# Kernel tuning notes

Hardware: AMD Instinct MI355X
Metric: run time of the kernel (lower is better)

The kernel has to match this reference:

```python
import jax, jax.numpy as jnp
import numpy as np

N_NODES = 500_000
N_EDGES = 2_500_000
N_GRAPHS = 1024


def _linear_params(key, fan_in, fan_out):
    # mimic torch.nn.Linear default init: U(-1/sqrt(fan_in), 1/sqrt(fan_in))
    k1, k2 = jax.random.split(key)
    bound = 1.0 / np.sqrt(fan_in)
    W = jax.random.uniform(k1, (fan_in, fan_out), jnp.float32, -bound, bound)
    b = jax.random.uniform(k2, (fan_out,), jnp.float32, -bound, bound)
    return W, b


def setup_inputs() -> dict:
    key = jax.random.key(0)
    ks = jax.random.split(key, 8)
    x = jax.random.normal(ks[0], (N_NODES, 2), jnp.float32)
    edge_index = jax.random.randint(ks[1], (2, N_EDGES), 0, N_NODES, jnp.int32)
    batch = jnp.sort(jax.random.randint(ks[2], (N_NODES,), 0, N_GRAPHS, jnp.int32))
    W1, b1 = _linear_params(ks[3], 2, 16)
    W2, b2 = _linear_params(ks[4], 16, 32)
    Wf1, bf1 = _linear_params(ks[5], 32, 16)
    Wf2, bf2 = _linear_params(ks[6], 16, 1)
    return {"x": x, "edge_index": edge_index, "batch": batch,
            "W1": W1, "b1": b1, "W2": W2, "b2": b2,
            "Wf1": Wf1, "bf1": bf1, "Wf2": Wf2, "bf2": bf2}


def _gnn_conv(h, W, b, src, dst, n_nodes):
    # Linear then add-aggregate: out[dst] += h_lin[src]  (self-loops already in src/dst)
    h = h @ W + b                       # [N, out]
    msgs = h[src]                       # gather over edges: [E+N, out]
    return jax.ops.segment_sum(msgs, dst, num_segments=n_nodes)


def reference(x, edge_index, batch, W1, b1, W2, b2, Wf1, bf1, Wf2, bf2):
    n = x.shape[0]
    loop = jnp.arange(n, dtype=edge_index.dtype)
    src = jnp.concatenate([edge_index[0], loop])  # source nodes (x_j)
    dst = jnp.concatenate([edge_index[1], loop])  # target nodes (aggregation index)

    h = jax.nn.relu(_gnn_conv(x, W1, b1, src, dst, n))   # [N, 16]
    h = jax.nn.relu(_gnn_conv(h, W2, b2, src, dst, n))   # [N, 32]

    # global mean pool per graph
    sums = jax.ops.segment_sum(h, batch, num_segments=N_GRAPHS)           # [G, 32]
    cnts = jax.ops.segment_sum(jnp.ones((n, 1), h.dtype), batch, num_segments=N_GRAPHS)
    pooled = sums / jnp.maximum(cnts, 1.0)

    out = jax.nn.relu(pooled @ Wf1 + bf1)
    out = out @ Wf2 + bf2                                # [G, 1]
    return out
```

## Files before the change

### kernel.cpp

```cpp
#include <hip/hip_runtime.h>


#define TPB 256
#define SBK_BITS 9
#define SBK 512
#define NSBX 1024
#define CAPX 576
#define CAPS 3072
#define PE1 4096

typedef unsigned int uint32;

__device__ __forceinline__ float reluf(float v) { return v > 0.f ? v : 0.f; }

__global__ void kPart1(const int* __restrict__ src, const int* __restrict__ dst,
                       int* __restrict__ curx, int* __restrict__ part1x, int E) {
    __shared__ int h[NSBX];
    for (int i = threadIdx.x; i < NSBX; i += TPB) h[i] = 0;
    __syncthreads();
    int base = blockIdx.x * PE1;
    int end = base + PE1 < E ? base + PE1 : E;
    for (int e = base + threadIdx.x; e < end; e += TPB)
        atomicAdd(&h[dst[e] >> SBK_BITS], 1);
    __syncthreads();
    int slice = blockIdx.x & 7;
    int* cur = curx + slice * NSBX;
    int rbase = slice * (NSBX * CAPX);
    for (int i = threadIdx.x; i < NSBX; i += TPB) {
        int c = h[i];
        if (c) h[i] = i * CAPX + atomicAdd(&cur[i], c);
    }
    __syncthreads();
    for (int e = base + threadIdx.x; e < end; e += TPB) {
        int d = dst[e];
        int b = d >> SBK_BITS;
        int pos = atomicAdd(&h[b], 1);
        if (pos < (b + 1) * CAPX)
            part1x[rbase + pos] = (src[e] << SBK_BITS) | (d & (SBK - 1));
    }
}

__global__ void kPart2C1(const int* __restrict__ curx, const int* __restrict__ part1x,
                         const float* __restrict__ x,
                         int* __restrict__ rowptr, int* __restrict__ supEnd,
                         int* __restrict__ partS, uint2* __restrict__ ninfo, int N) {
    __shared__ int hist[SBK];
    __shared__ int ps[TPB];
    __shared__ int sls[CAPS];
    __shared__ int segc[8];
    int sb = blockIdx.x;
    int node0 = sb << SBK_BITS;
    int sbase = sb * CAPS;
    int t = threadIdx.x;
    for (int i = t; i < SBK; i += TPB) hist[i] = 0;
    if (t < 8) {
        int c = curx[t * NSBX + sb];
        segc[t] = c > CAPX ? CAPX : c;
    }
    __syncthreads();
    for (int seg = 0; seg < 8; seg++) {
        const int* p = part1x + seg * (NSBX * CAPX) + sb * CAPX;
        int c = segc[seg];
        for (int i = t; i < c; i += TPB)
            atomicAdd(&hist[p[i] & (SBK - 1)], 1);
    }
    __syncthreads();
    int v0 = hist[2 * t], v1 = hist[2 * t + 1];
    int s = v0 + v1;
    ps[t] = s;
    __syncthreads();
    for (int off = 1; off < TPB; off <<= 1) {
        int u = (t >= off) ? ps[t - off] : 0;
        __syncthreads();
        ps[t] += u;
        __syncthreads();
    }
    int start0 = ps[t] - s;
    int start1 = start0 + v0;
    int n0 = node0 + 2 * t, n1 = n0 + 1;
    if (n0 < N) rowptr[n0] = sbase + start0;
    if (n1 < N) rowptr[n1] = sbase + start1;
    hist[2 * t] = start0;
    hist[2 * t + 1] = start1;
    if (t == TPB - 1) supEnd[sb] = sbase + ps[t];
    __syncthreads();
    for (int seg = 0; seg < 8; seg++) {
        const int* p = part1x + seg * (NSBX * CAPX) + sb * CAPX;
        int c = segc[seg];
        for (int i = t; i < c; i += TPB) {
            int w = p[i];
            int slot = atomicAdd(&hist[w & (SBK - 1)], 1);
            if (slot < CAPS) {
                int sid = w >> SBK_BITS;
                partS[sbase + slot] = sid;
                sls[slot] = sid;
            }
        }
    }
    __syncthreads();
#pragma unroll
    for (int half = 0; half < 2; half++) {
        int n = half ? n1 : n0;
        if (n >= N) continue;
        int st = half ? start1 : start0;
        int dg = half ? v1 : v0;
        int en = st + dg; if (en > CAPS) en = CAPS;
        float2 sv = ((const float2*)x)[n];
        float a0 = sv.x, a1 = sv.y;
        for (int e = st; e < en; e++) {
            float2 xv = ((const float2*)x)[sls[e]];
            a0 += xv.x; a1 += xv.y;
        }
        int indeg = dg + 1;
        if (indeg > 31) indeg = 31;
        ninfo[n] = make_uint2(__float_as_uint(a0),
                              (__float_as_uint(a1) & ~31u) | (uint32)indeg);
    }
}

__device__ __forceinline__ int rowEnd(const int* __restrict__ rowptr,
                                      const int* __restrict__ supEnd, int i, int N) {
    int nxt = i + 1;
    return (nxt >= N || (nxt & (SBK - 1)) == 0) ? supEnd[i >> SBK_BITS] : rowptr[nxt];
}

__device__ __forceinline__ void addMsg(float* a, uint2 q,
                                       const float* __restrict__ W1,
                                       const float* __restrict__ b1) {
    float n0 = __uint_as_float(q.x);
    float ndeg = (float)(q.y & 31u);
    float n1 = __uint_as_float(q.y & ~31u);
#pragma unroll
    for (int j = 0; j < 16; j++)
        a[j] += reluf(fmaf(n0, W1[j], fmaf(n1, W1[16 + j], ndeg * b1[j])));
}

__global__ void __launch_bounds__(TPB, 4)
kConv2(const uint2* __restrict__ ninfo, const int* __restrict__ partS,
       const int* __restrict__ rowptr, const int* __restrict__ supEnd,
       const int* __restrict__ batch,
       const float* __restrict__ W1, const float* __restrict__ b1,
       const float* __restrict__ W2, const float* __restrict__ b2,
       float* __restrict__ pooled, int N) {
    __shared__ float srow[TPB * 33];
    __shared__ int sbat[TPB];
    __shared__ float spart[8 * 32];
    int node0 = blockIdx.x * TPB;
    int l = threadIdx.x;
    int i = node0 + l;
    bool valid = i < N;

    if (valid) {
        int rs = rowptr[i];
        int re = rowEnd(rowptr, supEnd, i, N);
        uint2 p = ninfo[i];
        float s0 = __uint_as_float(p.x);
        float sdeg = (float)(p.y & 31u);
        float s1 = __uint_as_float(p.y & ~31u);
        float a[16];
#pragma unroll
        for (int j = 0; j < 16; j++)
            a[j] = reluf(fmaf(s0, W1[j], fmaf(s1, W1[16 + j], sdeg * b1[j])));
        int e = rs;
        for (; e + 4 <= re; e += 4) {
            int w0 = partS[e], w1 = partS[e + 1], w2 = partS[e + 2], w3 = partS[e + 3];
            uint2 q0 = ninfo[w0], q1 = ninfo[w1], q2 = ninfo[w2], q3 = ninfo[w3];
            addMsg(a, q0, W1, b1);
            addMsg(a, q1, W1, b1);
            addMsg(a, q2, W1, b1);
            addMsg(a, q3, W1, b1);
        }
        for (; e < re; e++)
            addMsg(a, ninfo[partS[e]], W1, b1);
#pragma unroll
        for (int j = 0; j < 32; j++) {
            float vv = sdeg * b2[j];
#pragma unroll
            for (int k = 0; k < 16; k++) vv = fmaf(a[k], W2[k * 32 + j], vv);
            srow[l * 33 + j] = reluf(vv);
        }
        sbat[l] = batch[i];
    } else {
#pragma unroll
        for (int j = 0; j < 32; j++) srow[l * 33 + j] = 0.f;
        sbat[l] = -1;
    }
    __syncthreads();
    int lastl = N - 1 - node0;
    if (lastl > TPB - 1) lastl = TPB - 1;
    int g0 = sbat[0], g1 = sbat[lastl];
    int f = threadIdx.x & 31, rr = threadIdx.x >> 5;
    for (int g = g0; g <= g1; g++) {
        float p = 0.f;
#pragma unroll 4
        for (int q = 0; q < 32; q++) {
            int n = rr + 8 * q;
            p += (sbat[n] == g) ? srow[n * 33 + f] : 0.f;
        }
        spart[rr * 32 + f] = p;
        __syncthreads();
        if (rr == 0) {
            float tot = 0.f;
#pragma unroll
            for (int q = 0; q < 8; q++) tot += spart[q * 32 + f];
            unsafeAtomicAdd(&pooled[32 * (size_t)g + f], tot);
        }
        __syncthreads();
    }
}

__device__ __forceinline__ int lower_bound(const int* __restrict__ a, int n, int v) {
    int lo = 0, hi = n;
    while (lo < hi) {
        int m = (lo + hi) >> 1;
        if (a[m] < v) lo = m + 1; else hi = m;
    }
    return lo;
}

__global__ void kMLP(const float* __restrict__ pooled, const int* __restrict__ batch,
                     const float* __restrict__ Wf1, const float* __restrict__ bf1,
                     const float* __restrict__ Wf2, const float* __restrict__ bf2,
                     float* __restrict__ out, int N, int G) {
    int g = blockIdx.x * blockDim.x + threadIdx.x;
    if (g >= G) return;
    int lo = lower_bound(batch, N, g);
    int hi = lower_bound(batch, N, g + 1);
    int cnt = hi - lo;
    float inv = 1.f / (float)(cnt > 1 ? cnt : 1);
    float p[32];
#pragma unroll
    for (int i = 0; i < 32; i++) p[i] = pooled[32 * (size_t)g + i] * inv;
    float acc = bf2[0];
#pragma unroll
    for (int j = 0; j < 16; j++) {
        float v = bf1[j];
#pragma unroll
        for (int i = 0; i < 32; i++) v = fmaf(p[i], Wf1[i * 16 + j], v);
        acc = fmaf(reluf(v), Wf2[j], acc);
    }
    out[g] = acc;
}

static inline size_t align256(size_t v) { return (v + 255) & ~(size_t)255; }

extern "C" void kernel_launch(void* const* d_in, const int* in_sizes, int n_in,
                              void* d_out, int out_size, void* d_ws, size_t ws_size,
                              hipStream_t stream) {
    const float* x    = (const float*)d_in[0];
    const int*   ei   = (const int*)d_in[1];
    const int*   batch= (const int*)d_in[2];
    const float* W1   = (const float*)d_in[3];
    const float* b1   = (const float*)d_in[4];
    const float* W2   = (const float*)d_in[5];
    const float* b2   = (const float*)d_in[6];
    const float* Wf1  = (const float*)d_in[7];
    const float* bf1  = (const float*)d_in[8];
    const float* Wf2  = (const float*)d_in[9];
    const float* bf2  = (const float*)d_in[10];
    float* out = (float*)d_out;

    const int N = in_sizes[0] / 2;
    const int E = in_sizes[1] / 2;
    const int G = out_size;
    const int* src = ei;
    const int* dst = ei + E;

    const int NSB = (N + SBK - 1) >> SBK_BITS;
    const int NFB = (N + TPB - 1) / TPB;

    char* w = (char*)d_ws;
    int*   curx   = (int*)w;    w += align256((size_t)8 * NSBX * sizeof(int));
    int*   supEnd = (int*)w;    w += align256((size_t)NSBX * sizeof(int));
    int*   rowptr = (int*)w;    w += align256((size_t)N * sizeof(int));
    uint2* ninfo  = (uint2*)w;  w += align256((size_t)N * sizeof(uint2));
    float* pooled = (float*)w;  w += align256((size_t)G * 32 * sizeof(float));
    int*   part1x = (int*)w;    w += align256((size_t)8 * NSBX * CAPX * sizeof(int));
    int*   partS  = (int*)w;    w += align256((size_t)NSBX * CAPS * sizeof(int));

    const int nb1 = (E + PE1 - 1) / PE1;

    hipMemsetAsync(curx, 0, (size_t)8 * NSBX * sizeof(int), stream);
    hipMemsetAsync(pooled, 0, (size_t)G * 32 * sizeof(float), stream);
    kPart1  <<<nb1, TPB, 0, stream>>>(src, dst, curx, part1x, E);
    kPart2C1<<<NSB, TPB, 0, stream>>>(curx, part1x, x, rowptr, supEnd, partS, ninfo, N);
    kConv2  <<<NFB, TPB, 0, stream>>>(ninfo, partS, rowptr, supEnd, batch,
                                      W1, b1, W2, b2, pooled, N);
    kMLP    <<<(G + TPB - 1) / TPB, TPB, 0, stream>>>(pooled, batch, Wf1, bf1, Wf2, bf2, out, N, G);
}
```

Measured before the change: 199.6 us.

## Split conv2 pooling into two 16-feature halves and fold pooled zeroing into partition kernel

The conv2 kernel now computes and pools the 32 output features in two halves of 16. This halves the shared-memory row buffer so the launch bounds can request 8 blocks per CU instead of 4. The separate memset of the pooled buffer is removed and its zeroing moved into the second partition kernel, which saves one launch. The trade-off is a second pooling pass with extra syncthreads, atomics issued in two halves, and a possible register-pressure or spill risk from the higher occupancy target.

New measurement: 233.4 us. 1.17x slower.

```diff
diff --git a/kernel.cpp b/kernel.cpp
--- a/kernel.cpp
+++ b/kernel.cpp
@@ -43,7 +43,11 @@
 __global__ void kPart2C1(const int* __restrict__ curx, const int* __restrict__ part1x,
                          const float* __restrict__ x,
                          int* __restrict__ rowptr, int* __restrict__ supEnd,
-                         int* __restrict__ partS, uint2* __restrict__ ninfo, int N) {
+                         int* __restrict__ partS, uint2* __restrict__ ninfo,
+                         float* __restrict__ pooled, int N, int G) {
+    int z = blockIdx.x * TPB + threadIdx.x;
+    if (z < 32 * G) pooled[z] = 0.f;
+
     __shared__ int hist[SBK];
     __shared__ int ps[TPB];
     __shared__ int sls[CAPS];
@@ -135,29 +139,29 @@
         a[j] += reluf(fmaf(n0, W1[j], fmaf(n1, W1[16 + j], ndeg * b1[j])));
 }
 
-__global__ void __launch_bounds__(TPB, 4)
+__global__ void __launch_bounds__(TPB, 8)
 kConv2(const uint2* __restrict__ ninfo, const int* __restrict__ partS,
        const int* __restrict__ rowptr, const int* __restrict__ supEnd,
        const int* __restrict__ batch,
        const float* __restrict__ W1, const float* __restrict__ b1,
        const float* __restrict__ W2, const float* __restrict__ b2,
        float* __restrict__ pooled, int N) {
-    __shared__ float srow[TPB * 33];
+    __shared__ float srow[TPB * 17];
     __shared__ int sbat[TPB];
-    __shared__ float spart[8 * 32];
+    __shared__ float spart[16 * 16];
     int node0 = blockIdx.x * TPB;
     int l = threadIdx.x;
     int i = node0 + l;
     bool valid = i < N;
-
+    float a[16];
+    float sdeg = 0.f;
     if (valid) {
         int rs = rowptr[i];
         int re = rowEnd(rowptr, supEnd, i, N);
         uint2 p = ninfo[i];
         float s0 = __uint_as_float(p.x);
-        float sdeg = (float)(p.y & 31u);
+        sdeg = (float)(p.y & 31u);
         float s1 = __uint_as_float(p.y & ~31u);
-        float a[16];
 #pragma unroll
         for (int j = 0; j < 16; j++)
             a[j] = reluf(fmaf(s0, W1[j], fmaf(s1, W1[16 + j], sdeg * b1[j])));
@@ -172,38 +176,49 @@
         }
         for (; e < re; e++)
             addMsg(a, ninfo[partS[e]], W1, b1);
-#pragma unroll
-        for (int j = 0; j < 32; j++) {
-            float vv = sdeg * b2[j];
-#pragma unroll
-            for (int k = 0; k < 16; k++) vv = fmaf(a[k], W2[k * 32 + j], vv);
-            srow[l * 33 + j] = reluf(vv);
-        }
         sbat[l] = batch[i];
     } else {
 #pragma unroll
-        for (int j = 0; j < 32; j++) srow[l * 33 + j] = 0.f;
+        for (int j = 0; j < 16; j++) a[j] = 0.f;
         sbat[l] = -1;
     }
     __syncthreads();
     int lastl = N - 1 - node0;
     if (lastl > TPB - 1) lastl = TPB - 1;
     int g0 = sbat[0], g1 = sbat[lastl];
-    int f = threadIdx.x & 31, rr = threadIdx.x >> 5;
-    for (int g = g0; g <= g1; g++) {
-        float p = 0.f;
-#pragma unroll 4
-        for (int q = 0; q < 32; q++) {
-            int n = rr + 8 * q;
-            p += (sbat[n] == g) ? srow[n * 33 + f] : 0.f;
-        }
-        spart[rr * 32 + f] = p;
+    int f = l & 15, rr = l >> 4;
+#pragma unroll
+    for (int h = 0; h < 2; h++) {
+        if (valid) {
+#pragma unroll
+            for (int jj = 0; jj < 16; jj++) {
+                int j = h * 16 + jj;
+                float vv = sdeg * b2[j];
+#pragma unroll
+                for (int k = 0; k < 16; k++) vv = fmaf(a[k], W2[k * 32 + j], vv);
+                srow[l * 17 + jj] = reluf(vv);
+            }
+        } else {
+#pragma unroll
+            for (int jj = 0; jj < 16; jj++) srow[l * 17 + jj] = 0.f;
+        }
         __syncthreads();
-        if (rr == 0) {
-            float tot = 0.f;
-#pragma unroll
-            for (int q = 0; q < 8; q++) tot += spart[q * 32 + f];
-            unsafeAtomicAdd(&pooled[32 * (size_t)g + f], tot);
+        for (int g = g0; g <= g1; g++) {
+            float p = 0.f;
+#pragma unroll
+            for (int q = 0; q < 16; q++) {
+                int n = rr + 16 * q;
+                p += (sbat[n] == g) ? srow[n * 17 + f] : 0.f;
+            }
+            spart[rr * 16 + f] = p;
+            __syncthreads();
+            if (rr == 0) {
+                float tot = 0.f;
+#pragma unroll
+                for (int q = 0; q < 16; q++) tot += spart[q * 16 + f];
+                unsafeAtomicAdd(&pooled[32 * (size_t)g + h * 16 + f], tot);
+            }
+            __syncthreads();
         }
         __syncthreads();
     }
@@ -281,9 +296,9 @@
     const int nb1 = (E + PE1 - 1) / PE1;
 
     hipMemsetAsync(curx, 0, (size_t)8 * NSBX * sizeof(int), stream);
-    hipMemsetAsync(pooled, 0, (size_t)G * 32 * sizeof(float), stream);
     kPart1  <<<nb1, TPB, 0, stream>>>(src, dst, curx, part1x, E);
-    kPart2C1<<<NSB, TPB, 0, stream>>>(curx, part1x, x, rowptr, supEnd, partS, ninfo, N);
+    kPart2C1<<<NSB, TPB, 0, stream>>>(curx, part1x, x, rowptr, supEnd, partS,
+                                      ninfo, pooled, N, G);
     kConv2  <<<NFB, TPB, 0, stream>>>(ninfo, partS, rowptr, supEnd, batch,
                                       W1, b1, W2, b2, pooled, N);
     kMLP    <<<(G + TPB - 1) / TPB, TPB, 0, stream>>>(pooled, batch, Wf1, bf1, Wf2, bf2, out, N, G);
```
